# Optimization experiments

Hardware: AMD Instinct MI355X
Metric: run time of the kernel (lower is better)

The kernel has to match this reference:

```python
import jax, jax.numpy as jnp
import numpy as np

D_IN = 1024
D_OUT = 1024
NUM_HEADS = 16
HEAD_DIM = D_OUT // NUM_HEADS


def setup_inputs() -> dict:
    key = jax.random.key(0)
    k1, k2, k3, k4 = jax.random.split(key, 4)
    x = jax.random.normal(k1, (2, 2048, D_IN), dtype=jnp.float32)
    # Linear weights stored torch-style [out_features, in_features]
    W_qkv = jax.random.normal(k2, (3 * D_OUT, D_IN), dtype=jnp.float32) * (1.0 / np.sqrt(D_IN))
    W_out = jax.random.normal(k3, (D_OUT, D_OUT), dtype=jnp.float32) * (1.0 / np.sqrt(D_OUT))
    b_out = jax.random.normal(k4, (D_OUT,), dtype=jnp.float32) * 0.01
    return {"x": x, "W_qkv": W_qkv, "W_out": W_out, "b_out": b_out}


def reference(x, W_qkv, W_out, b_out):
    b, s, _ = x.shape
    qkv = jnp.einsum('bsi,oi->bso', x, W_qkv)  # [b, s, 3*d_out]
    q, k, v = jnp.split(qkv, 3, axis=-1)
    def to_heads(t):
        return t.reshape(b, s, NUM_HEADS, HEAD_DIM).transpose(0, 2, 1, 3)
    q, k, v = to_heads(q), to_heads(k), to_heads(v)
    # NOTE: original module does NOT scale by 1/sqrt(head_dim)
    scores = jnp.einsum('bhqd,bhkd->bhqk', q, k)
    causal = jnp.tril(jnp.ones((s, s), dtype=bool))  # True = keep
    scores = jnp.where(causal[None, None], scores, -jnp.inf)
    attn = jax.nn.softmax(scores, axis=-1)
    ctx = jnp.einsum('bhqk,bhkd->bhqd', attn, v)
    ctx = ctx.transpose(0, 2, 1, 3).reshape(b, s, D_OUT)
    return jnp.einsum('bso,po->bsp', ctx, W_out) + b_out
```

## Files before the change

kernel.cpp:

```cpp
#include <hip/hip_runtime.h>
#include <cstdint>
#include <cstddef>


typedef __attribute__((ext_vector_type(8))) short bf16x8;
typedef __attribute__((ext_vector_type(4))) float f32x4;

#define LOG2E 1.44269504f

#define MFMA16(a, b, c) __builtin_amdgcn_mfma_f32_16x16x32_bf16((a), (b), (c), 0, 0, 0)

#define GLDS16(g, s)                                                        \
  __builtin_amdgcn_global_load_lds(                                         \
      (const __attribute__((address_space(1))) void*)(g),                   \
      (__attribute__((address_space(3))) void*)(s), 16, 0, 0)

#define ASYNC_BAR(N) asm volatile("s_waitcnt vmcnt(" #N ")\n\ts_barrier" ::: "memory")

#if __has_builtin(__builtin_amdgcn_exp2f)
#define EXP2F(x) __builtin_amdgcn_exp2f(x)
#else
#define EXP2F(x) exp2f(x)
#endif

static __device__ __forceinline__ unsigned short f2bf(float f) {
  unsigned int u = __builtin_bit_cast(unsigned int, f);
  u += 0x7FFFu + ((u >> 16) & 1u);
  return (unsigned short)(u >> 16);
}

static __device__ __forceinline__ unsigned int pk2bf(float a, float b) {
  const unsigned int ua = __builtin_bit_cast(unsigned int, a) + 0x8000u;
  const unsigned int ub = __builtin_bit_cast(unsigned int, b) + 0x8000u;
  return __builtin_amdgcn_perm(ub, ua, 0x07060302);
}

__global__ __launch_bounds__(256) void cast_bf16(const float* __restrict__ x,
                                                 const float* __restrict__ wq,
                                                 const float* __restrict__ wo,
                                                 unsigned short* __restrict__ xb,
                                                 unsigned short* __restrict__ wqb,
                                                 unsigned short* __restrict__ wob)
{
  const int id = blockIdx.x * 256 + threadIdx.x;
  const float* src;
  unsigned short* dst;
  int off;
  if (id < 1048576)               { src = x;  dst = xb;  off = id; }
  else if (id < 1048576 + 786432) { src = wq; dst = wqb; off = id - 1048576; }
  else                            { src = wo; dst = wob; off = id - (1048576 + 786432); }
  float4 v = ((const float4*)src)[off];
  ushort4 o;
  o.x = f2bf(v.x); o.y = f2bf(v.y); o.z = f2bf(v.z); o.w = f2bf(v.w);
  ((ushort4*)dst)[off] = o;
}

template <int MODE>
__global__ __launch_bounds__(256) void gemm_bt(const unsigned short* __restrict__ A,
                                               const unsigned short* __restrict__ B,
                                               const float* __restrict__ bias,
                                               float* __restrict__ OutF,
                                               unsigned short* __restrict__ Qb,
                                               unsigned short* __restrict__ Kb,
                                               unsigned short* __restrict__ Vt)
{
  __shared__ unsigned short pool[24576];

  const int tid  = threadIdx.x;
  const int wave = tid >> 6, lane = tid & 63, quad = lane >> 4, cl = lane & 15;
  const int wm = wave >> 1, wn = wave & 1;
  const int m0 = blockIdx.y * 128, n0 = blockIdx.x * 128;
  const int sr = lane >> 2, sc = lane & 3;

  const int part = (MODE == 1) ? (n0 >> 10) : 0;
  const bool swapped = (MODE == 0) || (part < 2);

  f32x4 acc[4][4];
  #pragma unroll
  for (int i = 0; i < 4; ++i)
    #pragma unroll
    for (int j = 0; j < 4; ++j)
      #pragma unroll
      for (int r = 0; r < 4; ++r) acc[i][j][r] = 0.f;

  const int scs = (sc ^ ((sr >> 1) & 3)) * 8;
  const int rchunk = (quad ^ ((cl >> 1) & 3)) * 8;

  auto stage = [&](int k0, int buf) {
    unsigned short* As = pool + buf * 8192;
    unsigned short* Bs = As + 4096;
    #pragma unroll
    for (int ii = 0; ii < 2; ++ii) {
      const int r = wave * 32 + ii * 16 + sr;
      GLDS16(A + (size_t)(m0 + r) * 1024 + k0 + scs, &As[(wave * 32 + ii * 16) * 32]);
      GLDS16(B + (size_t)(n0 + r) * 1024 + k0 + scs, &Bs[(wave * 32 + ii * 16) * 32]);
    }
  };

  stage(0, 0);
  stage(32, 1);
  int cur = 0;
  #pragma unroll 1
  for (int it = 0; it < 32; ++it) {
    if (it + 2 < 32) {
      ASYNC_BAR(4);
      const int bnx = (cur == 0) ? 2 : cur - 1;
      stage((it + 2) * 32, bnx);
    } else if (it + 1 < 32) {
      ASYNC_BAR(4);
    } else {
      ASYNC_BAR(0);
    }

    const unsigned short* As = pool + cur * 8192;
    const unsigned short* Bs = As + 4096;
    bf16x8 af[4], bfr[4];
    #pragma unroll
    for (int mt = 0; mt < 4; ++mt)
      af[mt] = *(const bf16x8*)&As[(wm * 64 + mt * 16 + cl) * 32 + rchunk];
    #pragma unroll
    for (int nt = 0; nt < 4; ++nt)
      bfr[nt] = *(const bf16x8*)&Bs[(wn * 64 + nt * 16 + cl) * 32 + rchunk];

    if (swapped) {
      #pragma unroll
      for (int mt = 0; mt < 4; ++mt)
        #pragma unroll
        for (int nt = 0; nt < 4; ++nt)
          acc[mt][nt] = MFMA16(bfr[nt], af[mt], acc[mt][nt]);
    } else {
      #pragma unroll
      for (int mt = 0; mt < 4; ++mt)
        #pragma unroll
        for (int nt = 0; nt < 4; ++nt)
          acc[mt][nt] = MFMA16(af[mt], bfr[nt], acc[mt][nt]);
    }
    cur = (cur == 2) ? 0 : cur + 1;
  }

  if (MODE == 1) {
    const int bb = m0 >> 11, ss = m0 & 2047;
    if (part == 2) {
      #pragma unroll
      for (int half = 0; half < 2; ++half) {
        __syncthreads();
        if (wn == half) {
          #pragma unroll
          for (int mt = 0; mt < 4; ++mt)
            #pragma unroll
            for (int nt = 0; nt < 4; ++nt) {
              const int nl = nt * 16 + cl;
              const int ml = wm * 64 + mt * 16 + quad * 4;
              ushort4 pk;
              pk.x = f2bf(acc[mt][nt][0]); pk.y = f2bf(acc[mt][nt][1]);
              pk.z = f2bf(acc[mt][nt][2]); pk.w = f2bf(acc[mt][nt][3]);
              *(ushort4*)&pool[nl * 136 + ml] = pk;
            }
        }
        __syncthreads();
        const int row = tid >> 2, q4 = tid & 3;
        const int nglob = n0 + half * 64 + row;
        const int hh = (nglob >> 6) & 15, d = nglob & 63;
        unsigned short* drow = Vt + ((size_t)(bb * 16 + hh) * 64 + d) * 2048 + ss;
        #pragma unroll
        for (int i = 0; i < 4; ++i) {
          const bf16x8 v = *(const bf16x8*)&pool[row * 136 + q4 * 32 + i * 8];
          *(bf16x8*)(drow + q4 * 32 + i * 8) = v;
        }
      }
    } else {
      unsigned short* dst = (part == 0) ? Qb : Kb;
      const float sc2 = (part == 0) ? LOG2E : 1.0f;
      #pragma unroll
      for (int mt = 0; mt < 4; ++mt) {
        const int m = ss + wm * 64 + mt * 16 + cl;
        #pragma unroll
        for (int nt = 0; nt < 4; ++nt) {
          const int np = (n0 & 1023) + wn * 64 + nt * 16 + quad * 4;
          const int hh = np >> 6, d0 = np & 63;
          ushort4 pk;
          pk.x = f2bf(acc[mt][nt][0] * sc2);
          pk.y = f2bf(acc[mt][nt][1] * sc2);
          pk.z = f2bf(acc[mt][nt][2] * sc2);
          pk.w = f2bf(acc[mt][nt][3] * sc2);
          *(ushort4*)&dst[((size_t)(bb * 16 + hh) * 2048 + m) * 64 + d0] = pk;
        }
      }
    }
  } else {
    #pragma unroll
    for (int mt = 0; mt < 4; ++mt) {
      const int m = m0 + wm * 64 + mt * 16 + cl;
      #pragma unroll
      for (int nt = 0; nt < 4; ++nt) {
        const int n = n0 + wn * 64 + nt * 16 + quad * 4;
        const float4 bv = *(const float4*)(bias + n);
        float4 o;
        o.x = acc[mt][nt][0] + bv.x; o.y = acc[mt][nt][1] + bv.y;
        o.z = acc[mt][nt][2] + bv.z; o.w = acc[mt][nt][3] + bv.w;
        *(float4*)&OutF[(size_t)m * 1024 + n] = o;
      }
    }
  }
}

__global__ __launch_bounds__(256) void attn_mfma(const unsigned short* __restrict__ Qb,
                                                 const unsigned short* __restrict__ Kb,
                                                 const unsigned short* __restrict__ Vt,
                                                 unsigned short* __restrict__ CTX)
{
  __shared__ unsigned short Ksm[3][64 * 64];
  __shared__ unsigned short Vsm[3][64 * 64];
  __shared__ unsigned short Psm[4][32 * 40];

  const int tid  = threadIdx.x;
  const int wave = tid >> 6, lane = tid & 63, quad = lane >> 4, cl = lane & 15;

  const int L  = blockIdx.x;
  const int bh = 4 * (L & 7) + ((L >> 3) & 3);
  const int b  = bh >> 4, h = bh & 15;
  const int p  = L >> 5;
  const int g  = p * 4 + wave;
  const int qlo = g * 16;
  const int qhi = (127 - g) * 16;
  const size_t base = (size_t)bh * (2048 * 64);

  bf16x8 qf[2][2];
  #pragma unroll
  for (int dk = 0; dk < 2; ++dk) {
    qf[0][dk] = *(const bf16x8*)(Qb + base + (size_t)(qlo + cl) * 64 + dk * 32 + quad * 8);
    qf[1][dk] = *(const bf16x8*)(Qb + base + (size_t)(qhi + cl) * 64 + dk * 32 + quad * 8);
  }

  f32x4 oacc[2][4];
  #pragma unroll
  for (int mf = 0; mf < 2; ++mf)
    #pragma unroll
    for (int dt = 0; dt < 4; ++dt)
      #pragma unroll
      for (int r = 0; r < 4; ++r) oacc[mf][dt][r] = 0.f;
  float lr[2][4] = {};

  bf16x8 ones;
  #pragma unroll
  for (int k = 0; k < 8; ++k) ones[k] = (short)0x3F80;

  const int lrow  = lane >> 3;
  const int lslot = (lane & 7) ^ lrow;
  const int nch = 32 - p;

  auto stageKV = [&](int j64, int buf) {
    #pragma unroll
    for (int ii = 0; ii < 2; ++ii) {
      const int r0 = wave * 16 + ii * 8;
      GLDS16(Kb + base + (size_t)(j64 + r0 + lrow) * 64 + lslot * 8, &Ksm[buf][r0 * 64]);
      GLDS16(Vt + base + (size_t)(r0 + lrow) * 2048 + j64 + lslot * 8, &Vsm[buf][r0 * 64]);
    }
  };

  stageKV(0, 0);
  stageKV(64, 1);
  int cur = 0;
  #pragma unroll 1
  for (int ch = 0; ch < nch; ++ch) {
    if (ch + 2 < nch) {
      ASYNC_BAR(4);
      const int bnx = (cur == 0) ? 2 : cur - 1;
      stageKV((ch + 2) * 64, bnx);
    } else if (ch + 1 < nch) {
      ASYNC_BAR(4);
    } else {
      ASYNC_BAR(0);
    }

    const int j64 = ch * 64;
    #pragma unroll
    for (int jli = 0; jli < 2; ++jli) {
      const int jg0 = j64 + jli * 32;
      if (jg0 > qhi + 15) continue;
      const bool lowAct = (jg0 <= qlo + 15);
      const int jl = jli * 32;

      bf16x8 kf[2][2];
      #pragma unroll
      for (int jf = 0; jf < 2; ++jf)
        #pragma unroll
        for (int dk = 0; dk < 2; ++dk) {
          const int jrow = jl + jf * 16 + cl;
          const int slot = (dk * 4 + quad) ^ (cl & 7);
          kf[jf][dk] = *(const bf16x8*)&Ksm[cur][jrow * 64 + slot * 8];
        }

      f32x4 st[2][2];
      #pragma unroll
      for (int jf = 0; jf < 2; ++jf)
        #pragma unroll
        for (int mf = 0; mf < 2; ++mf) {
          if (mf == 0 && !lowAct) continue;
          f32x4 z;
          #pragma unroll
          for (int r = 0; r < 4; ++r) z[r] = 0.f;
          z = MFMA16(kf[jf][0], qf[mf][0], z);
          st[jf][mf] = MFMA16(kf[jf][1], qf[mf][1], z);
        }

      #pragma unroll
      for (int mf = 0; mf < 2; ++mf) {
        if (mf == 0 && !lowAct) continue;
        const int qbase = mf ? qhi : qlo;
        const bool diag = (jg0 + 32 > qbase);
        #pragma unroll
        for (int jf = 0; jf < 2; ++jf) {
          float pv[4];
          if (diag) {
            const int qg = qbase + cl;
            #pragma unroll
            for (int r = 0; r < 4; ++r) {
              const int jg = jg0 + jf * 16 + quad * 4 + r;
              pv[r] = (jg <= qg) ? EXP2F(st[jf][mf][r]) : 0.f;
            }
          } else {
            #pragma unroll
            for (int r = 0; r < 4; ++r) pv[r] = EXP2F(st[jf][mf][r]);
          }
          uint2 w;
          w.x = pk2bf(pv[0], pv[1]);
          w.y = pk2bf(pv[2], pv[3]);
          *(uint2*)&Psm[wave][(mf * 16 + cl) * 40 + jf * 16 + quad * 4] = w;
        }
      }

      bf16x8 vf[4];
      #pragma unroll
      for (int dt = 0; dt < 4; ++dt) {
        const int d = dt * 16 + cl;
        const int slot = ((jl >> 3) + quad) ^ (cl & 7);
        vf[dt] = *(const bf16x8*)&Vsm[cur][d * 64 + slot * 8];
      }

      #pragma unroll
      for (int mf = 0; mf < 2; ++mf) {
        if (mf == 0 && !lowAct) continue;
        const bf16x8 pf = *(const bf16x8*)&Psm[wave][(mf * 16 + cl) * 40 + quad * 8];
        f32x4 z;
        #pragma unroll
        for (int r = 0; r < 4; ++r) z[r] = 0.f;
        const f32x4 ls = MFMA16(pf, ones, z);
        #pragma unroll
        for (int r = 0; r < 4; ++r) lr[mf][r] += ls[r];
        #pragma unroll
        for (int dt = 0; dt < 4; ++dt)
          oacc[mf][dt] = MFMA16(pf, vf[dt], oacc[mf][dt]);
      }
    }
    cur = (cur == 2) ? 0 : cur + 1;
  }

  #pragma unroll
  for (int mf = 0; mf < 2; ++mf) {
    const int qbase = mf ? qhi : qlo;
    float inv[4];
    #pragma unroll
    for (int r = 0; r < 4; ++r) inv[r] = 1.f / lr[mf][r];
    #pragma unroll
    for (int dt = 0; dt < 4; ++dt)
      #pragma unroll
      for (int r = 0; r < 4; ++r)
        CTX[(size_t)(b * 2048 + qbase + quad * 4 + r) * 1024 +
            h * 64 + dt * 16 + cl] = f2bf(oacc[mf][dt][r] * inv[r]);
  }
}

extern "C" void kernel_launch(void* const* d_in, const int* in_sizes, int n_in,
                              void* d_out, int out_size, void* d_ws, size_t ws_size,
                              hipStream_t stream)
{
  const float* x    = (const float*)d_in[0];
  const float* Wqkv = (const float*)d_in[1];
  const float* Wout = (const float*)d_in[2];
  const float* bout = (const float*)d_in[3];
  float* out = (float*)d_out;

  char* ws = (char*)d_ws;
  unsigned short* xb  = (unsigned short*)(ws);
  unsigned short* wqb = (unsigned short*)(ws + 8388608);
  unsigned short* wob = (unsigned short*)(ws + 14680064);
  unsigned short* Qb  = (unsigned short*)(ws + 16777216);
  unsigned short* Kb  = (unsigned short*)(ws + 25165824);
  unsigned short* Vt  = (unsigned short*)(ws + 33554432);
  unsigned short* CTX = (unsigned short*)(ws + 41943040);

  cast_bf16<<<dim3(8192), dim3(256), 0, stream>>>(x, Wqkv, Wout, xb, wqb, wob);

  gemm_bt<1><<<dim3(24, 32), dim3(256), 0, stream>>>(xb, wqb, nullptr, nullptr, Qb, Kb, Vt);

  attn_mfma<<<dim3(512), dim3(256), 0, stream>>>(Qb, Kb, Vt, CTX);

  gemm_bt<0><<<dim3(8, 32), dim3(256), 0, stream>>>(CTX, wob, bout, out, nullptr, nullptr, nullptr);
}
```

Before: 196.5 us.

## Split output GEMM into narrower tiles and shrink attention KV chunks to 32

The output-projection GEMM becomes its own kernel with a 128x64 tile, so the grid doubles from 256 to 512 blocks and fills the GPU's compute units better. The attention kernel now stages 32-key chunks instead of 64, with smaller LDS buffers, a new V swizzle and twice as many pipeline iterations. Less LDS per block may allow higher occupancy in attention. The cost is more barriers and loop overhead per key, plus less B-tile reuse in the output GEMM.

```diff
diff --git a/kernel.cpp b/kernel.cpp
--- a/kernel.cpp
+++ b/kernel.cpp
@@ -55,14 +55,11 @@
   ((ushort4*)dst)[off] = o;
 }
 
-template <int MODE>
-__global__ __launch_bounds__(256) void gemm_bt(const unsigned short* __restrict__ A,
-                                               const unsigned short* __restrict__ B,
-                                               const float* __restrict__ bias,
-                                               float* __restrict__ OutF,
-                                               unsigned short* __restrict__ Qb,
-                                               unsigned short* __restrict__ Kb,
-                                               unsigned short* __restrict__ Vt)
+__global__ __launch_bounds__(256) void gemm_qkv(const unsigned short* __restrict__ A,
+                                                const unsigned short* __restrict__ B,
+                                                unsigned short* __restrict__ Qb,
+                                                unsigned short* __restrict__ Kb,
+                                                unsigned short* __restrict__ Vt)
 {
   __shared__ unsigned short pool[24576];
 
@@ -72,8 +69,8 @@
   const int m0 = blockIdx.y * 128, n0 = blockIdx.x * 128;
   const int sr = lane >> 2, sc = lane & 3;
 
-  const int part = (MODE == 1) ? (n0 >> 10) : 0;
-  const bool swapped = (MODE == 0) || (part < 2);
+  const int part = n0 >> 10;
+  const bool swapped = (part < 2);
 
   f32x4 acc[4][4];
   #pragma unroll
@@ -138,68 +135,136 @@
     cur = (cur == 2) ? 0 : cur + 1;
   }
 
-  if (MODE == 1) {
-    const int bb = m0 >> 11, ss = m0 & 2047;
-    if (part == 2) {
-      #pragma unroll
-      for (int half = 0; half < 2; ++half) {
-        __syncthreads();
-        if (wn == half) {
+  const int bb = m0 >> 11, ss = m0 & 2047;
+  if (part == 2) {
+    #pragma unroll
+    for (int half = 0; half < 2; ++half) {
+      __syncthreads();
+      if (wn == half) {
+        #pragma unroll
+        for (int mt = 0; mt < 4; ++mt)
           #pragma unroll
-          for (int mt = 0; mt < 4; ++mt)
-            #pragma unroll
-            for (int nt = 0; nt < 4; ++nt) {
-              const int nl = nt * 16 + cl;
-              const int ml = wm * 64 + mt * 16 + quad * 4;
-              ushort4 pk;
-              pk.x = f2bf(acc[mt][nt][0]); pk.y = f2bf(acc[mt][nt][1]);
-              pk.z = f2bf(acc[mt][nt][2]); pk.w = f2bf(acc[mt][nt][3]);
-              *(ushort4*)&pool[nl * 136 + ml] = pk;
-            }
-        }
-        __syncthreads();
-        const int row = tid >> 2, q4 = tid & 3;
-        const int nglob = n0 + half * 64 + row;
-        const int hh = (nglob >> 6) & 15, d = nglob & 63;
-        unsigned short* drow = Vt + ((size_t)(bb * 16 + hh) * 64 + d) * 2048 + ss;
-        #pragma unroll
-        for (int i = 0; i < 4; ++i) {
-          const bf16x8 v = *(const bf16x8*)&pool[row * 136 + q4 * 32 + i * 8];
-          *(bf16x8*)(drow + q4 * 32 + i * 8) = v;
-        }
-      }
+          for (int nt = 0; nt < 4; ++nt) {
+            const int nl = nt * 16 + cl;
+            const int ml = wm * 64 + mt * 16 + quad * 4;
+            ushort4 pk;
+            pk.x = f2bf(acc[mt][nt][0]); pk.y = f2bf(acc[mt][nt][1]);
+            pk.z = f2bf(acc[mt][nt][2]); pk.w = f2bf(acc[mt][nt][3]);
+            *(ushort4*)&pool[nl * 136 + ml] = pk;
+          }
+      }
+      __syncthreads();
+      const int row = tid >> 2, q4 = tid & 3;
+      const int nglob = n0 + half * 64 + row;
+      const int hh = (nglob >> 6) & 15, d = nglob & 63;
+      unsigned short* drow = Vt + ((size_t)(bb * 16 + hh) * 64 + d) * 2048 + ss;
+      #pragma unroll
+      for (int i = 0; i < 4; ++i) {
+        const bf16x8 v = *(const bf16x8*)&pool[row * 136 + q4 * 32 + i * 8];
+        *(bf16x8*)(drow + q4 * 32 + i * 8) = v;
+      }
+    }
+  } else {
+    unsigned short* dst = (part == 0) ? Qb : Kb;
+    const float sc2 = (part == 0) ? LOG2E : 1.0f;
+    #pragma unroll
+    for (int mt = 0; mt < 4; ++mt) {
+      const int m = ss + wm * 64 + mt * 16 + cl;
+      #pragma unroll
+      for (int nt = 0; nt < 4; ++nt) {
+        const int np = (n0 & 1023) + wn * 64 + nt * 16 + quad * 4;
+        const int hh = np >> 6, d0 = np & 63;
+        ushort4 pk;
+        pk.x = f2bf(acc[mt][nt][0] * sc2);
+        pk.y = f2bf(acc[mt][nt][1] * sc2);
+        pk.z = f2bf(acc[mt][nt][2] * sc2);
+        pk.w = f2bf(acc[mt][nt][3] * sc2);
+        *(ushort4*)&dst[((size_t)(bb * 16 + hh) * 2048 + m) * 64 + d0] = pk;
+      }
+    }
+  }
+}
+
+__global__ __launch_bounds__(256) void gemm_out(const unsigned short* __restrict__ A,
+                                                const unsigned short* __restrict__ B,
+                                                const float* __restrict__ bias,
+                                                float* __restrict__ OutF)
+{
+  __shared__ unsigned short pool[18432];
+
+  const int tid  = threadIdx.x;
+  const int wave = tid >> 6, lane = tid & 63, quad = lane >> 4, cl = lane & 15;
+  const int wm = wave >> 1, wn = wave & 1;
+  const int m0 = blockIdx.y * 128, n0 = blockIdx.x * 64;
+  const int sr = lane >> 2, sc = lane & 3;
+
+  f32x4 acc[4][2];
+  #pragma unroll
+  for (int i = 0; i < 4; ++i)
+    #pragma unroll
+    for (int j = 0; j < 2; ++j)
+      #pragma unroll
+      for (int r = 0; r < 4; ++r) acc[i][j][r] = 0.f;
+
+  const int scs = (sc ^ ((sr >> 1) & 3)) * 8;
+  const int rchunk = (quad ^ ((cl >> 1) & 3)) * 8;
+
+  auto stage = [&](int k0, int buf) {
+    unsigned short* As = pool + buf * 6144;
+    unsigned short* Bs = As + 4096;
+    #pragma unroll
+    for (int ii = 0; ii < 2; ++ii) {
+      const int r = wave * 32 + ii * 16 + sr;
+      GLDS16(A + (size_t)(m0 + r) * 1024 + k0 + scs, &As[(wave * 32 + ii * 16) * 32]);
+    }
+    const int rb = wave * 16 + sr;
+    GLDS16(B + (size_t)(n0 + rb) * 1024 + k0 + scs, &Bs[wave * 16 * 32]);
+  };
+
+  stage(0, 0);
+  stage(32, 1);
+  int cur = 0;
+  #pragma unroll 1
+  for (int it = 0; it < 32; ++it) {
+    if (it + 2 < 32) {
+      ASYNC_BAR(3);
+      const int bnx = (cur == 0) ? 2 : cur - 1;
+      stage((it + 2) * 32, bnx);
+    } else if (it + 1 < 32) {
+      ASYNC_BAR(3);
     } else {
-      unsigned short* dst = (part == 0) ? Qb : Kb;
-      const float sc2 = (part == 0) ? LOG2E : 1.0f;
-      #pragma unroll
-      for (int mt = 0; mt < 4; ++mt) {
-        const int m = ss + wm * 64 + mt * 16 + cl;
-        #pragma unroll
-        for (int nt = 0; nt < 4; ++nt) {
-          const int np = (n0 & 1023) + wn * 64 + nt * 16 + quad * 4;
-          const int hh = np >> 6, d0 = np & 63;
-          ushort4 pk;
-          pk.x = f2bf(acc[mt][nt][0] * sc2);
-          pk.y = f2bf(acc[mt][nt][1] * sc2);
-          pk.z = f2bf(acc[mt][nt][2] * sc2);
-          pk.w = f2bf(acc[mt][nt][3] * sc2);
-          *(ushort4*)&dst[((size_t)(bb * 16 + hh) * 2048 + m) * 64 + d0] = pk;
-        }
-      }
-    }
-  } else {
-    #pragma unroll
-    for (int mt = 0; mt < 4; ++mt) {
-      const int m = m0 + wm * 64 + mt * 16 + cl;
-      #pragma unroll
-      for (int nt = 0; nt < 4; ++nt) {
-        const int n = n0 + wn * 64 + nt * 16 + quad * 4;
-        const float4 bv = *(const float4*)(bias + n);
-        float4 o;
-        o.x = acc[mt][nt][0] + bv.x; o.y = acc[mt][nt][1] + bv.y;
-        o.z = acc[mt][nt][2] + bv.z; o.w = acc[mt][nt][3] + bv.w;
-        *(float4*)&OutF[(size_t)m * 1024 + n] = o;
-      }
+      ASYNC_BAR(0);
+    }
+
+    const unsigned short* As = pool + cur * 6144;
+    const unsigned short* Bs = As + 4096;
+    bf16x8 af[4], bfr[2];
+    #pragma unroll
+    for (int mt = 0; mt < 4; ++mt)
+      af[mt] = *(const bf16x8*)&As[(wm * 64 + mt * 16 + cl) * 32 + rchunk];
+    #pragma unroll
+    for (int nt = 0; nt < 2; ++nt)
+      bfr[nt] = *(const bf16x8*)&Bs[(wn * 32 + nt * 16 + cl) * 32 + rchunk];
+
+    #pragma unroll
+    for (int mt = 0; mt < 4; ++mt)
+      #pragma unroll
+      for (int nt = 0; nt < 2; ++nt)
+        acc[mt][nt] = MFMA16(bfr[nt], af[mt], acc[mt][nt]);
+    cur = (cur == 2) ? 0 : cur + 1;
+  }
+
+  #pragma unroll
+  for (int mt = 0; mt < 4; ++mt) {
+    const int m = m0 + wm * 64 + mt * 16 + cl;
+    #pragma unroll
+    for (int nt = 0; nt < 2; ++nt) {
+      const int n = n0 + wn * 32 + nt * 16 + quad * 4;
+      const float4 bv = *(const float4*)(bias + n);
+      float4 o;
+      o.x = acc[mt][nt][0] + bv.x; o.y = acc[mt][nt][1] + bv.y;
+      o.z = acc[mt][nt][2] + bv.z; o.w = acc[mt][nt][3] + bv.w;
+      *(float4*)&OutF[(size_t)m * 1024 + n] = o;
     }
   }
 }
@@ -209,8 +274,8 @@
                                                  const unsigned short* __restrict__ Vt,
                                                  unsigned short* __restrict__ CTX)
 {
-  __shared__ unsigned short Ksm[3][64 * 64];
-  __shared__ unsigned short Vsm[3][64 * 64];
+  __shared__ unsigned short Ksm[3][32 * 64];
+  __shared__ unsigned short Vsm[3][64 * 32];
   __shared__ unsigned short Psm[4][32 * 40];
 
   const int tid  = threadIdx.x;
@@ -245,50 +310,46 @@
   #pragma unroll
   for (int k = 0; k < 8; ++k) ones[k] = (short)0x3F80;
 
-  const int lrow  = lane >> 3;
-  const int lslot = (lane & 7) ^ lrow;
-  const int nch = 32 - p;
-
-  auto stageKV = [&](int j64, int buf) {
-    #pragma unroll
-    for (int ii = 0; ii < 2; ++ii) {
-      const int r0 = wave * 16 + ii * 8;
-      GLDS16(Kb + base + (size_t)(j64 + r0 + lrow) * 64 + lslot * 8, &Ksm[buf][r0 * 64]);
-      GLDS16(Vt + base + (size_t)(r0 + lrow) * 2048 + j64 + lslot * 8, &Vsm[buf][r0 * 64]);
-    }
+  const int krow  = lane >> 3;
+  const int kslot = (lane & 7) ^ krow;
+  const int vrow  = lane >> 2;
+  const int vslot = (lane & 3) ^ (vrow & 3);
+
+  const int nch = 64 - 2 * p;
+
+  auto stageKV = [&](int j32, int buf) {
+    GLDS16(Kb + base + (size_t)(j32 + wave * 8 + krow) * 64 + kslot * 8,
+           &Ksm[buf][wave * 8 * 64]);
+    GLDS16(Vt + base + (size_t)(wave * 16 + vrow) * 2048 + j32 + vslot * 8,
+           &Vsm[buf][wave * 16 * 32]);
   };
 
   stageKV(0, 0);
-  stageKV(64, 1);
+  stageKV(32, 1);
   int cur = 0;
   #pragma unroll 1
   for (int ch = 0; ch < nch; ++ch) {
     if (ch + 2 < nch) {
-      ASYNC_BAR(4);
+      ASYNC_BAR(2);
       const int bnx = (cur == 0) ? 2 : cur - 1;
-      stageKV((ch + 2) * 64, bnx);
+      stageKV((ch + 2) * 32, bnx);
     } else if (ch + 1 < nch) {
-      ASYNC_BAR(4);
+      ASYNC_BAR(2);
     } else {
       ASYNC_BAR(0);
     }
 
-    const int j64 = ch * 64;
-    #pragma unroll
-    for (int jli = 0; jli < 2; ++jli) {
-      const int jg0 = j64 + jli * 32;
-      if (jg0 > qhi + 15) continue;
+    const int jg0 = ch * 32;
+    if (jg0 <= qhi + 15) {
       const bool lowAct = (jg0 <= qlo + 15);
-      const int jl = jli * 32;
 
       bf16x8 kf[2][2];
       #pragma unroll
       for (int jf = 0; jf < 2; ++jf)
         #pragma unroll
         for (int dk = 0; dk < 2; ++dk) {
-          const int jrow = jl + jf * 16 + cl;
           const int slot = (dk * 4 + quad) ^ (cl & 7);
-          kf[jf][dk] = *(const bf16x8*)&Ksm[cur][jrow * 64 + slot * 8];
+          kf[jf][dk] = *(const bf16x8*)&Ksm[cur][(jf * 16 + cl) * 64 + slot * 8];
         }
 
       f32x4 st[2][2];
@@ -334,8 +395,8 @@
       #pragma unroll
       for (int dt = 0; dt < 4; ++dt) {
         const int d = dt * 16 + cl;
-        const int slot = ((jl >> 3) + quad) ^ (cl & 7);
-        vf[dt] = *(const bf16x8*)&Vsm[cur][d * 64 + slot * 8];
+        const int slot = quad ^ (cl & 3);
+        vf[dt] = *(const bf16x8*)&Vsm[cur][d * 32 + slot * 8];
       }
 
       #pragma unroll
@@ -392,9 +453,9 @@
 
   cast_bf16<<<dim3(8192), dim3(256), 0, stream>>>(x, Wqkv, Wout, xb, wqb, wob);
 
-  gemm_bt<1><<<dim3(24, 32), dim3(256), 0, stream>>>(xb, wqb, nullptr, nullptr, Qb, Kb, Vt);
+  gemm_qkv<<<dim3(24, 32), dim3(256), 0, stream>>>(xb, wqb, Qb, Kb, Vt);
 
   attn_mfma<<<dim3(512), dim3(256), 0, stream>>>(Qb, Kb, Vt, CTX);
 
-  gemm_bt<0><<<dim3(8, 32), dim3(256), 0, stream>>>(CTX, wob, bout, out, nullptr, nullptr, nullptr);
-}
+  gemm_out<<<dim3(16, 32), dim3(256), 0, stream>>>(CTX, wob, bout, out);
+}
```

Result: slower. 209.3 us (+6.5%).
